# Performance work log

Measured on AMD Instinct MI355X. Metric: run time of the kernel, lower is better.

The kernel has to match this reference:

```python
import jax, jax.numpy as jnp
import numpy as np

T_STEPS = 100
T_EMB = 16
EPS = 1e-8


def sin_emb(t, dim):
    # sinusoidal_time_embedding: [cos(t*f), sin(t*f)] with f = exp(-log(1e4)*i/half)
    half = dim // 2
    freqs = jnp.exp(-jnp.log(jnp.float32(10000.0)) * jnp.arange(half, dtype=jnp.float32) / half)
    a = t.astype(jnp.float32)[:, None] * freqs[None, :]
    return jnp.concatenate([jnp.cos(a), jnp.sin(a)], axis=-1)


def lstm_layer(x_tbf, W_ih, W_hh, b):
    # x_tbf: [T, B, F]; torch gate order i, f, g, o
    B = x_tbf.shape[1]
    H = W_hh.shape[1]

    def step(carry, x_t):
        h, c = carry
        g = x_t @ W_ih.T + h @ W_hh.T + b
        i, f, gg, o = jnp.split(g, 4, axis=-1)
        c = jax.nn.sigmoid(f) * c + jax.nn.sigmoid(i) * jnp.tanh(gg)
        h = jax.nn.sigmoid(o) * jnp.tanh(c)
        return (h, c), h

    z = jnp.zeros((B, H), x_tbf.dtype)
    (h, c), ys = jax.lax.scan(step, (z, z), x_tbf)
    return ys, h


def _forward(x_hist, x_future, y0, turb_idx, pred_steps, init_noise, turb_emb,
             W_ih0, W_hh0, b_ih0, b_hh0, W_ih1, W_hh1, b_ih1, b_hh1,
             W1, b1, W2, b2, W3, b3):
    betas = jnp.linspace(1e-4, 0.02, T_STEPS).astype(jnp.float32)
    alphas = 1.0 - betas
    alpha_bars = jnp.cumprod(alphas)

    B = x_hist.shape[0]
    emb = turb_emb[turb_idx]  # [B, E]
    eh = jnp.broadcast_to(emb[:, None, :], (B, x_hist.shape[1], emb.shape[1]))
    ef = jnp.broadcast_to(emb[:, None, :], (B, x_future.shape[1], emb.shape[1]))
    xh = jnp.concatenate([x_hist, eh], axis=-1).transpose(1, 0, 2)    # [T_in, B, F+E]
    xf = jnp.concatenate([x_future, ef], axis=-1).transpose(1, 0, 2)  # [P, B, exo+E]

    ys0, _ = lstm_layer(xh, W_ih0, W_hh0, b_ih0 + b_hh0)
    _, enc_out = lstm_layer(ys0, W_ih1, W_hh1, b_ih1 + b_hh1)         # [B, H] = h[-1]

    def mlp(x):
        h = jax.nn.relu(x @ W1.T + b1)
        h = jax.nn.relu(h @ W2.T + b2)
        return h @ W3.T + b3

    def ar_step(prev_y, xs):
        exo_t, step, y_init = xs
        cond = jnp.concatenate([enc_out, exo_t, prev_y], axis=1)  # [B, cond_dim]
        h_e = sin_emb(jnp.full((B,), step), T_EMB)

        def dstep(y, t):
            t_e = sin_emb(jnp.full((B,), t), T_EMB)
            eps_hat = mlp(jnp.concatenate([cond, y, t_e, h_e], axis=1))  # [B,1]
            b_t, a_t, ab_t = betas[t], alphas[t], alpha_bars[t]
            pred_x0 = (y - jnp.sqrt(1.0 - ab_t) * eps_hat) / (jnp.sqrt(ab_t) + EPS)
            mean = (y - b_t / (jnp.sqrt(1.0 - ab_t) + EPS) * eps_hat) / (jnp.sqrt(a_t) + EPS)
            # eval mode -> deterministic sampling: posterior noise term is zero
            return jnp.where(t == 0, pred_x0, mean), None

        y, _ = jax.lax.scan(dstep, y_init, jnp.arange(T_STEPS - 1, -1, -1))
        return y, y[:, 0]

    _, seq = jax.lax.scan(ar_step, y0, (xf, jnp.arange(pred_steps), init_noise))
    return seq.T[:, :, None]  # [B, pred_steps, 1]


def setup_inputs() -> dict:
    key = jax.random.key(0)
    ks = list(jax.random.split(key, 24))
    kit = iter(ks)
    B, T_IN, F_IN, EXO, EMB, PRED, HID, NTURB = 1024, 96, 8, 6, 16, 8, 128, 100
    in0 = F_IN + EMB                 # 24
    cond_dim = HID + EXO + EMB + 1   # 151
    in_mlp = cond_dim + 1 + T_EMB + T_EMB  # 184

    def nrm(shape, s=0.05):
        return jax.random.normal(next(kit), shape, jnp.float32) * s

    return {
        'x_hist': jax.random.normal(next(kit), (B, T_IN, F_IN), jnp.float32),
        'x_future': jax.random.normal(next(kit), (B, PRED, EXO), jnp.float32),
        'y0': jnp.zeros((B, 1), jnp.float32),
        'turb_idx': jax.random.randint(next(kit), (B,), 0, NTURB),
        'pred_steps': PRED,
        'init_noise': jax.random.normal(next(kit), (PRED, B, 1), jnp.float32),
        'turb_emb': nrm((NTURB, EMB), 0.1),
        'W_ih0': nrm((4 * HID, in0)), 'W_hh0': nrm((4 * HID, HID)),
        'b_ih0': jnp.zeros((4 * HID,), jnp.float32), 'b_hh0': jnp.zeros((4 * HID,), jnp.float32),
        'W_ih1': nrm((4 * HID, HID)), 'W_hh1': nrm((4 * HID, HID)),
        'b_ih1': jnp.zeros((4 * HID,), jnp.float32), 'b_hh1': jnp.zeros((4 * HID,), jnp.float32),
        'W1': nrm((HID, in_mlp)), 'b1': jnp.zeros((HID,), jnp.float32),
        'W2': nrm((HID, HID)), 'b2': jnp.zeros((HID,), jnp.float32),
        'W3': nrm((1, HID)), 'b3': jnp.zeros((1,), jnp.float32),
    }


def reference(x_hist, x_future, y0, turb_idx, pred_steps, init_noise, turb_emb,
              W_ih0, W_hh0, b_ih0, b_hh0, W_ih1, W_hh1, b_ih1, b_hh1,
              W1, b1, W2, b2, W3, b3):
    return _forward(x_hist, x_future, y0, turb_idx, pred_steps, init_noise, turb_emb,
                    W_ih0, W_hh0, b_ih0, b_hh0, W_ih1, W_hh1, b_ih1, b_hh1,
                    W1, b1, W2, b2, W3, b3)
```

## Files before the change

kernel.cpp:

```cpp
#include <hip/hip_runtime.h>
#include <hip/hip_fp16.h>
#include <stdint.h>


typedef __attribute__((ext_vector_type(2))) _Float16 half2_t;
typedef __attribute__((ext_vector_type(8))) _Float16 v8h;
typedef __attribute__((ext_vector_type(4))) float v4f;

#define DEV __device__ __forceinline__

DEV uint32_t pack2f(float a, float b) {
  __half ha = __float2half_rn(a), hb = __float2half_rn(b);
  return (uint32_t)__half_as_ushort(ha) | ((uint32_t)__half_as_ushort(hb) << 16);
}

DEV float2 up2(uint32_t u) {
  half2_t h = __builtin_bit_cast(half2_t, u);
  return make_float2((float)h.x, (float)h.y);
}

DEV float fast_ex2(float x) {
#if __has_builtin(__builtin_amdgcn_exp2f)
  return __builtin_amdgcn_exp2f(x);
#else
  return exp2f(x);
#endif
}
DEV float fast_rcp(float x) {
#if __has_builtin(__builtin_amdgcn_rcpf)
  return __builtin_amdgcn_rcpf(x);
#else
  return 1.f / x;
#endif
}
DEV float sigm(float x) { return fast_rcp(1.f + fast_ex2(-1.4426950408889634f * x)); }
DEV float tanh_f(float x) {
  return 2.f * fast_rcp(1.f + fast_ex2(-2.8853900817779268f * x)) - 1.f;
}

DEV uint32_t pk_add(uint32_t a, uint32_t b) {
  return __builtin_bit_cast(uint32_t,
      __builtin_bit_cast(half2_t, a) + __builtin_bit_cast(half2_t, b));
}

DEV uint32_t pk_relufma(uint32_t w, uint32_t y, uint32_t b) {
  half2_t r = __builtin_bit_cast(half2_t, w) * __builtin_bit_cast(half2_t, y) +
              __builtin_bit_cast(half2_t, b);
  half2_t z = {(_Float16)0.f, (_Float16)0.f};
#if __has_builtin(__builtin_elementwise_max)
  r = __builtin_elementwise_max(r, z);
#else
  uint32_t u = __builtin_bit_cast(uint32_t, r);
  uint32_t mask = ((u >> 15) & 1u) * 0xFFFFu | ((u >> 31) & 1u) * 0xFFFF0000u;
  r = __builtin_bit_cast(half2_t, u & ~mask);
#endif
  return __builtin_bit_cast(uint32_t, r);
}

DEV uint32_t cvtpk(float y) {
#if __has_builtin(__builtin_amdgcn_cvt_pkrtz)
  return __builtin_bit_cast(uint32_t, __builtin_amdgcn_cvt_pkrtz(y, y));
#else
  return pack2f(y, y);
#endif
}

DEV float rowsum16(float v) {
  int x;
  x = __builtin_amdgcn_update_dpp(0, __builtin_bit_cast(int, v), 0x111, 0xf, 0xf, true);
  v += __builtin_bit_cast(float, x);
  x = __builtin_amdgcn_update_dpp(0, __builtin_bit_cast(int, v), 0x112, 0xf, 0xf, true);
  v += __builtin_bit_cast(float, x);
  x = __builtin_amdgcn_update_dpp(0, __builtin_bit_cast(int, v), 0x114, 0xf, 0xf, true);
  v += __builtin_bit_cast(float, x);
  x = __builtin_amdgcn_update_dpp(0, __builtin_bit_cast(int, v), 0x118, 0xf, 0xf, true);
  v += __builtin_bit_cast(float, x);
  return v;
}

static constexpr size_t OFF_XH  = 0;
static constexpr size_t OFF_W0  = 4718592;
static constexpr size_t OFF_BS0 = 4882432;
static constexpr size_t OFF_W1L = 4884480;
static constexpr size_t OFF_BS1 = 5146624;
static constexpr size_t OFF_W2P = 5148672;
static constexpr size_t OFF_ENC = 5181440;
static constexpr size_t OFF_YS0 = 5705728;

__global__ void k_prep_xh(const float* __restrict__ xh, const int* __restrict__ tix,
                          const float* __restrict__ temb, uint32_t* __restrict__ out) {
  int idx = blockIdx.x * 256 + threadIdx.x;
  if (idx >= 96 * 1024 * 12) return;
  int m = idx % 12;
  int tb = idx / 12;
  int b = tb & 1023, t = tb >> 10;
  int k0 = 2 * m, k1 = k0 + 1;
  float v0 = (k0 < 8) ? xh[(b * 96 + t) * 8 + k0] : temb[tix[b] * 16 + (k0 - 8)];
  float v1 = (k1 < 8) ? xh[(b * 96 + t) * 8 + k1] : temb[tix[b] * 16 + (k1 - 8)];
  out[idx] = pack2f(v0, v1);
}

__global__ void k_prep_w(const float* __restrict__ Wih0, const float* __restrict__ Whh0,
                         const float* __restrict__ bih0, const float* __restrict__ bhh0,
                         const float* __restrict__ Wih1, const float* __restrict__ Whh1,
                         const float* __restrict__ bih1, const float* __restrict__ bhh1,
                         const float* __restrict__ W2,
                         uint32_t* __restrict__ w0p, uint32_t* __restrict__ w1p,
                         uint32_t* __restrict__ w2p, float* __restrict__ bs0,
                         float* __restrict__ bs1) {
  int idx = blockIdx.x * 256 + threadIdx.x;
  if (idx < 40960) {
    int w = idx / 5120;
    int r = idx % 5120;
    int T = r / 1280; r %= 1280;
    int f = r / 256;  r %= 256;
    int l = r >> 2, c = r & 3;
    int m = l & 15, qf = l >> 4;
    int g = (m & 3) * 128 + w * 16 + (m >> 2) * 4 + T;
    int k0 = f * 32 + qf * 8 + 2 * c, k1 = k0 + 1;
    float a = (k0 < 24) ? Wih0[g * 24 + k0] : ((k0 < 152) ? Whh0[g * 128 + k0 - 24] : 0.f);
    float b = (k1 < 24) ? Wih0[g * 24 + k1] : ((k1 < 152) ? Whh0[g * 128 + k1 - 24] : 0.f);
    w0p[idx] = pack2f(a, b);
  } else if (idx < 106496) {
    int i = idx - 40960;
    int w = i / 8192;
    int r = i % 8192;
    int T = r / 2048; r %= 2048;
    int f = r / 256;  r %= 256;
    int l = r >> 2, c = r & 3;
    int m = l & 15, qf = l >> 4;
    int g = (m & 3) * 128 + w * 16 + (m >> 2) * 4 + T;
    int k0 = f * 32 + qf * 8 + 2 * c, k1 = k0 + 1;
    float a = (k0 < 128) ? Wih1[g * 128 + k0] : Whh1[g * 128 + k0 - 128];
    float b = (k1 < 128) ? Wih1[g * 128 + k1] : Whh1[g * 128 + k1 - 128];
    w1p[i] = pack2f(a, b);
  } else if (idx < 114688) {
    int i = idx - 106496;
    w2p[i] = pack2f(W2[2 * i], W2[2 * i + 1]);
  } else if (idx < 115200) {
    int i = idx - 114688;
    bs0[i] = bih0[i] + bhh0[i];
  } else if (idx < 115712) {
    int i = idx - 115200;
    bs1[i] = bih1[i] + bhh1[i];
  }
}

__global__ __launch_bounds__(512, 2) void k_lstm0(const uint32_t* __restrict__ xh16,
                                                  const uint32_t* __restrict__ w0A,
                                                  const float* __restrict__ bs0,
                                                  __half* __restrict__ ys0) {
  __shared__ __align__(16) __half inb[2][16][160];
  const int tid = threadIdx.x;
  const int w = tid >> 6, l = tid & 63;
  const int n = l & 15, ql = l >> 4;
  const int ju = w * 16 + ql * 4;
  const int bbase = blockIdx.x * 16;

  uint4 Af[4][5];
#pragma unroll
  for (int T = 0; T < 4; T++)
#pragma unroll
    for (int f = 0; f < 5; f++)
      Af[T][f] = ((const uint4*)w0A)[((w * 4 + T) * 5 + f) * 64 + l];
  float bias[4][4];
#pragma unroll
  for (int T = 0; T < 4; T++)
#pragma unroll
    for (int r = 0; r < 4; r++) bias[T][r] = bs0[r * 128 + ju + T];

  for (int i = tid; i < 2560; i += 512) ((uint32_t*)inb)[i] = 0u;
  __syncthreads();
  if (tid < 192) {
    int b = tid / 12, m = tid % 12;
    ((uint32_t*)&inb[0][b][0])[m] = xh16[(0 * 1024 + bbase + b) * 12 + m];
  }
  float cst[4] = {0.f, 0.f, 0.f, 0.f};
  __syncthreads();

  for (int t = 0; t < 96; t++) {
    const int cur = t & 1, nxt = cur ^ 1;
    uint32_t sx = 0;
    int sb = 0, sm = 0;
    if (t < 95 && tid < 192) {
      sb = tid / 12; sm = tid % 12;
      sx = xh16[((t + 1) * 1024 + bbase + sb) * 12 + sm];
    }
    v4f acc[4];
#pragma unroll
    for (int T = 0; T < 4; T++) acc[T] = (v4f){0.f, 0.f, 0.f, 0.f};
#pragma unroll
    for (int f = 0; f < 5; f++) {
      uint4 bu = *(const uint4*)&inb[cur][n][f * 32 + ql * 8];
      v8h Bv = __builtin_bit_cast(v8h, bu);
#pragma unroll
      for (int T = 0; T < 4; T++)
        acc[T] = __builtin_amdgcn_mfma_f32_16x16x32_f16(
            __builtin_bit_cast(v8h, Af[T][f]), Bv, acc[T], 0, 0, 0);
    }
    float hv[4];
#pragma unroll
    for (int T = 0; T < 4; T++) {
      float gi = acc[T][0] + bias[T][0];
      float gf = acc[T][1] + bias[T][1];
      float gg = acc[T][2] + bias[T][2];
      float go = acc[T][3] + bias[T][3];
      float c = sigm(gf) * cst[T] + sigm(gi) * tanh_f(gg);
      cst[T] = c;
      hv[T] = sigm(go) * tanh_f(c);
    }
    uint32_t h01 = pack2f(hv[0], hv[1]), h23 = pack2f(hv[2], hv[3]);
    *(uint2*)&inb[nxt][n][24 + ju] = make_uint2(h01, h23);
    *(uint2*)((__half*)ys0 + (size_t)(t * 1024 + bbase + n) * 128 + ju) = make_uint2(h01, h23);
    if (t < 95 && tid < 192) ((uint32_t*)&inb[nxt][sb][0])[sm] = sx;
    __syncthreads();
  }
}

__global__ __launch_bounds__(512, 2) void k_lstm1(const uint32_t* __restrict__ ys0u,
                                                  const uint32_t* __restrict__ w1A,
                                                  const float* __restrict__ bs1,
                                                  float* __restrict__ enc) {
  __shared__ __align__(16) __half inb[2][16][264];
  const int tid = threadIdx.x;
  const int w = tid >> 6, l = tid & 63;
  const int n = l & 15, ql = l >> 4;
  const int ju = w * 16 + ql * 4;
  const int bbase = blockIdx.x * 16;
  const int sb = tid >> 5, sc = tid & 31;

  uint4 Af[4][8];
#pragma unroll
  for (int T = 0; T < 4; T++)
#pragma unroll
    for (int f = 0; f < 8; f++)
      Af[T][f] = ((const uint4*)w1A)[((w * 4 + T) * 8 + f) * 64 + l];
  float bias[4][4];
#pragma unroll
  for (int T = 0; T < 4; T++)
#pragma unroll
    for (int r = 0; r < 4; r++) bias[T][r] = bs1[r * 128 + ju + T];

  for (int i = tid; i < 4224; i += 512) ((uint32_t*)inb)[i] = 0u;
  __syncthreads();
  {
    uint2 v = ((const uint2*)ys0u)[(size_t)(0 * 1024 + bbase + sb) * 32 + sc];
    *(uint2*)&inb[0][sb][sc * 4] = v;
  }
  float cst[4] = {0.f, 0.f, 0.f, 0.f};
  __syncthreads();

  for (int t = 0; t < 96; t++) {
    const int cur = t & 1, nxt = cur ^ 1;
    uint2 sv = make_uint2(0u, 0u);
    if (t < 95)
      sv = ((const uint2*)ys0u)[(size_t)((t + 1) * 1024 + bbase + sb) * 32 + sc];
    v4f acc[4];
#pragma unroll
    for (int T = 0; T < 4; T++) acc[T] = (v4f){0.f, 0.f, 0.f, 0.f};
#pragma unroll
    for (int f = 0; f < 8; f++) {
      uint4 bu = *(const uint4*)&inb[cur][n][f * 32 + ql * 8];
      v8h Bv = __builtin_bit_cast(v8h, bu);
#pragma unroll
      for (int T = 0; T < 4; T++)
        acc[T] = __builtin_amdgcn_mfma_f32_16x16x32_f16(
            __builtin_bit_cast(v8h, Af[T][f]), Bv, acc[T], 0, 0, 0);
    }
    float hv[4];
#pragma unroll
    for (int T = 0; T < 4; T++) {
      float gi = acc[T][0] + bias[T][0];
      float gf = acc[T][1] + bias[T][1];
      float gg = acc[T][2] + bias[T][2];
      float go = acc[T][3] + bias[T][3];
      float c = sigm(gf) * cst[T] + sigm(gi) * tanh_f(gg);
      cst[T] = c;
      hv[T] = sigm(go) * tanh_f(c);
    }
    *(uint2*)&inb[nxt][n][128 + ju] = make_uint2(pack2f(hv[0], hv[1]), pack2f(hv[2], hv[3]));
    if (t < 95) *(uint2*)&inb[nxt][sb][sc * 4] = sv;
    if (t == 95)
      *(float4*)&enc[(size_t)(bbase + n) * 128 + ju] = make_float4(hv[0], hv[1], hv[2], hv[3]);
    __syncthreads();
  }
}

__global__ __launch_bounds__(256, 1) void k_diff(
    const float* __restrict__ xfut, const float* __restrict__ y0,
    const int* __restrict__ tix, const float* __restrict__ noise,
    const float* __restrict__ temb, const float* __restrict__ W1,
    const float* __restrict__ b1, const float* __restrict__ b2,
    const float* __restrict__ W3, const float* __restrict__ b3,
    const uint32_t* __restrict__ w2p, const float* __restrict__ enc,
    float* __restrict__ out) {
  __shared__ uint32_t W1sL[128 * 65];
  __shared__ uint32_t W1xL[128 * 29];
  __shared__ uint32_t encPL[16 * 65];
  __shared__ uint32_t embPL[16 * 9];
  __shared__ float teL[100][16];
  __shared__ float2 ccL[100];
  __shared__ __align__(16) __half tprojL[100 * 128];
  __shared__ __half hprojL[8 * 128];
  __shared__ __align__(16) float partL[2][4][16];
  __shared__ uint32_t encdL[256 * 17];

  const int tid = threadIdx.x;
  const int w = tid >> 6, l = tid & 63;
  const int m = l & 15, q = l >> 4;
  const int bbase = blockIdx.x * 16;

  for (int i = tid; i < 128 * 64; i += 256) {
    int r = i >> 6, c = i & 63;
    W1sL[r * 65 + c] = pack2f(W1[r * 184 + 2 * c], W1[r * 184 + 2 * c + 1]);
  }
  for (int i = tid; i < 128 * 28; i += 256) {
    int r = i / 28, c = i % 28;
    W1xL[r * 29 + c] = pack2f(W1[r * 184 + 128 + 2 * c], W1[r * 184 + 129 + 2 * c]);
  }
  for (int i = tid; i < 16 * 64; i += 256) {
    int bb = i >> 6, c = i & 63;
    encPL[bb * 65 + c] = pack2f(enc[(bbase + bb) * 128 + 2 * c],
                                enc[(bbase + bb) * 128 + 2 * c + 1]);
  }
  for (int i = tid; i < 16 * 8; i += 256) {
    int bb = i >> 3, c = i & 7;
    const float* er = temb + tix[bbase + bb] * 16;
    embPL[bb * 9 + c] = pack2f(er[2 * c], er[2 * c + 1]);
  }
  for (int p = tid; p < 1600; p += 256) {
    int tt = p >> 4, i = p & 15;
    float f = expf(-logf(10000.f) * (float)(i & 7) / 8.f);
    float a = (float)tt * f;
    teL[tt][i] = (i < 8) ? cosf(a) : sinf(a);
  }
  for (int qq = tid; qq < 100; qq += 256) {
    float ab = 1.f, beta = 0.f;
    for (int i = 0; i <= qq; i++) {
      beta = 1e-4f + (0.02f - 1e-4f) * (float)i / 99.f;
      ab *= (1.f - beta);
    }
    float cs, cd;
    if (qq == 0) { cs = sqrtf(1.f - ab); cd = 1.f / (sqrtf(ab) + 1e-8f); }
    else { cs = beta / (sqrtf(1.f - ab) + 1e-8f); cd = 1.f / (sqrtf(1.f - beta) + 1e-8f); }
    ccL[qq] = make_float2(cs, cd);
  }
  __syncthreads();

  {
    int k = tid & 127, hs = tid >> 7;
    float wte[16], whe[16];
#pragma unroll
    for (int i = 0; i < 8; i++) {
      float2 a = up2(W1xL[k * 29 + 12 + i]);
      wte[2 * i] = a.x; wte[2 * i + 1] = a.y;
      float2 bqq = up2(W1xL[k * 29 + 20 + i]);
      whe[2 * i] = bqq.x; whe[2 * i + 1] = bqq.y;
    }
    for (int tt = hs * 50; tt < hs * 50 + 50; tt++) {
      float s = 0.f;
#pragma unroll
      for (int i = 0; i < 16; i++) s += wte[i] * teL[tt][i];
      tprojL[tt * 128 + k] = __float2half_rn(s);
    }
    if (hs == 0) {
      for (int ss = 0; ss < 8; ss++) {
        float s = 0.f;
#pragma unroll
        for (int i = 0; i < 16; i++) s += whe[i] * teL[ss][i];
        hprojL[ss * 128 + k] = __float2half_rn(s);
      }
    }
  }

  for (int pi = 0; pi < 16; pi++) {
    int k0 = (pi >> 2) * 32 + q * 8 + (pi & 3) * 2;
    half2_t a0 = {(_Float16)0.f, (_Float16)0.f};
    half2_t a1 = a0;
    const uint32_t* wr0 = &W1sL[k0 * 65];
    const uint32_t* wr1 = &W1sL[(k0 + 1) * 65];
    const uint32_t* ep = &encPL[m * 65];
#pragma unroll 8
    for (int c = 0; c < 64; c++) {
      half2_t e = __builtin_bit_cast(half2_t, ep[c]);
      a0 += __builtin_bit_cast(half2_t, wr0[c]) * e;
      a1 += __builtin_bit_cast(half2_t, wr1[c]) * e;
    }
#pragma unroll
    for (int c = 0; c < 8; c++) {
      half2_t e = __builtin_bit_cast(half2_t, embPL[m * 9 + c]);
      a0 += __builtin_bit_cast(half2_t, W1xL[k0 * 29 + 3 + c]) * e;
      a1 += __builtin_bit_cast(half2_t, W1xL[(k0 + 1) * 29 + 3 + c]) * e;
    }
    float e0 = b1[k0] + (float)a0.x + (float)a0.y;
    float e1 = b1[k0 + 1] + (float)a1.x + (float)a1.y;
    encdL[tid * 17 + pi] = pack2f(e0, e1);
  }

  uint4 Bf[2][4];
  const uint4* w2u4 = (const uint4*)w2p;
#pragma unroll
  for (int tt = 0; tt < 2; tt++) {
    int n = w * 32 + tt * 16 + m;
#pragma unroll
    for (int f = 0; f < 4; f++) Bf[tt][f] = w2u4[n * 16 + f * 4 + q];
  }
  const float w3v0 = W3[w * 32 + m], w3v1 = W3[w * 32 + 16 + m];
  const float b2v0 = b2[w * 32 + m], b2v1 = b2[w * 32 + 16 + m];
  const float b3v = b3[0];

  uint32_t w1yP[16];
#pragma unroll
  for (int pi = 0; pi < 16; pi++) {
    int k0 = (pi >> 2) * 32 + q * 8 + (pi & 3) * 2;
    uint32_t ua = W1xL[k0 * 29 + 11];
    uint32_t ub = W1xL[(k0 + 1) * 29 + 11];
    w1yP[pi] = (ua >> 16) | (ub & 0xFFFF0000u);
  }

  float prev_y = y0[bbase + m];
  float noi[8];
#pragma unroll
  for (int s = 0; s < 8; s++) noi[s] = noise[s * 1024 + bbase + m];
  __syncthreads();

  int buf = 0;
  for (int s = 0; s < 8; s++) {
    float xf[6];
#pragma unroll
    for (int i = 0; i < 6; i++) xf[i] = xfut[((bbase + m) * 8 + s) * 6 + i];
    uint32_t bph[16];
#pragma unroll
    for (int pi = 0; pi < 16; pi++) {
      int k0 = (pi >> 2) * 32 + q * 8 + (pi & 3) * 2;
      float2 ed = up2(encdL[tid * 17 + pi]);
      float e0 = ed.x, e1 = ed.y;
#pragma unroll
      for (int c = 0; c < 3; c++) {
        float2 w0v = up2(W1xL[k0 * 29 + c]);
        float2 w1v = up2(W1xL[(k0 + 1) * 29 + c]);
        e0 += w0v.x * xf[2 * c] + w0v.y * xf[2 * c + 1];
        e1 += w1v.x * xf[2 * c] + w1v.y * xf[2 * c + 1];
      }
      e0 += up2(W1xL[k0 * 29 + 11]).x * prev_y;
      e1 += up2(W1xL[(k0 + 1) * 29 + 11]).x * prev_y;
      e0 += (float)hprojL[s * 128 + k0];
      e1 += (float)hprojL[s * 128 + k0 + 1];
      bph[pi] = pack2f(e0, e1);
    }

    float y = noi[s];
    uint32_t bt[16];
    {
      const uint4* tb = (const uint4*)(tprojL + 99 * 128 + q * 8);
      uint4 t0 = tb[0], t1 = tb[4], t2 = tb[8], t3 = tb[12];
      bt[0] = pk_add(bph[0], t0.x);  bt[1] = pk_add(bph[1], t0.y);
      bt[2] = pk_add(bph[2], t0.z);  bt[3] = pk_add(bph[3], t0.w);
      bt[4] = pk_add(bph[4], t1.x);  bt[5] = pk_add(bph[5], t1.y);
      bt[6] = pk_add(bph[6], t1.z);  bt[7] = pk_add(bph[7], t1.w);
      bt[8] = pk_add(bph[8], t2.x);  bt[9] = pk_add(bph[9], t2.y);
      bt[10] = pk_add(bph[10], t2.z); bt[11] = pk_add(bph[11], t2.w);
      bt[12] = pk_add(bph[12], t3.x); bt[13] = pk_add(bph[13], t3.y);
      bt[14] = pk_add(bph[14], t3.z); bt[15] = pk_add(bph[15], t3.w);
    }
    float2 ccv = ccL[99];

    for (int t = 99; t >= 0; t--) {
      uint32_t yP = cvtpk(y);
      v4f c0a = {0.f, 0.f, 0.f, 0.f}, c0b = c0a, c1a = c0a, c1b = c0a;
#pragma unroll
      for (int f = 0; f < 4; f++) {
        uint4 au;
        au.x = pk_relufma(w1yP[4 * f + 0], yP, bt[4 * f + 0]);
        au.y = pk_relufma(w1yP[4 * f + 1], yP, bt[4 * f + 1]);
        au.z = pk_relufma(w1yP[4 * f + 2], yP, bt[4 * f + 2]);
        au.w = pk_relufma(w1yP[4 * f + 3], yP, bt[4 * f + 3]);
        v8h A = __builtin_bit_cast(v8h, au);
        if (f & 1) {
          c0b = __builtin_amdgcn_mfma_f32_16x16x32_f16(A, __builtin_bit_cast(v8h, Bf[0][f]), c0b, 0, 0, 0);
          c1b = __builtin_amdgcn_mfma_f32_16x16x32_f16(A, __builtin_bit_cast(v8h, Bf[1][f]), c1b, 0, 0, 0);
        } else {
          c0a = __builtin_amdgcn_mfma_f32_16x16x32_f16(A, __builtin_bit_cast(v8h, Bf[0][f]), c0a, 0, 0, 0);
          c1a = __builtin_amdgcn_mfma_f32_16x16x32_f16(A, __builtin_bit_cast(v8h, Bf[1][f]), c1a, 0, 0, 0);
        }
      }
      const int tn = (t > 0) ? t - 1 : 0;
      const uint4* tb = (const uint4*)(tprojL + tn * 128 + q * 8);
      uint4 t0 = tb[0], t1 = tb[4], t2 = tb[8], t3 = tb[12];
      float2 ccn = ccL[tn];
      v4f c0 = c0a + c0b, c1 = c1a + c1b;
      float pr[4];
#pragma unroll
      for (int r = 0; r < 4; r++) {
        pr[r] = fmaxf(c0[r] + b2v0, 0.f) * w3v0 + fmaxf(c1[r] + b2v1, 0.f) * w3v1;
        pr[r] = rowsum16(pr[r]);
      }
      if ((l & 15) == 15)
        *(float4*)&partL[buf][w][q * 4] = make_float4(pr[0], pr[1], pr[2], pr[3]);
      uint32_t btn[16];
      btn[0] = pk_add(bph[0], t0.x);  btn[1] = pk_add(bph[1], t0.y);
      btn[2] = pk_add(bph[2], t0.z);  btn[3] = pk_add(bph[3], t0.w);
      btn[4] = pk_add(bph[4], t1.x);  btn[5] = pk_add(bph[5], t1.y);
      btn[6] = pk_add(bph[6], t1.z);  btn[7] = pk_add(bph[7], t1.w);
      btn[8] = pk_add(bph[8], t2.x);  btn[9] = pk_add(bph[9], t2.y);
      btn[10] = pk_add(bph[10], t2.z); btn[11] = pk_add(bph[11], t2.w);
      btn[12] = pk_add(bph[12], t3.x); btn[13] = pk_add(bph[13], t3.y);
      btn[14] = pk_add(bph[14], t3.z); btn[15] = pk_add(bph[15], t3.w);
      __syncthreads();
      float eps = b3v + ((partL[buf][0][m] + partL[buf][1][m]) +
                         (partL[buf][2][m] + partL[buf][3][m]));
      y = (y - ccv.x * eps) * ccv.y;
      ccv = ccn;
#pragma unroll
      for (int pi = 0; pi < 16; pi++) bt[pi] = btn[pi];
      buf ^= 1;
    }
    if (w == 0 && l < 16) out[(bbase + l) * 8 + s] = y;
    prev_y = y;
  }
}

extern "C" void kernel_launch(void* const* d_in, const int* in_sizes, int n_in,
                              void* d_out, int out_size, void* d_ws, size_t ws_size,
                              hipStream_t stream) {
  const float* x_hist    = (const float*)d_in[0];
  const float* x_future  = (const float*)d_in[1];
  const float* y0        = (const float*)d_in[2];
  const int*   turb_idx  = (const int*)d_in[3];
  const float* init_noise = (const float*)d_in[5];
  const float* turb_emb  = (const float*)d_in[6];
  const float* W_ih0     = (const float*)d_in[7];
  const float* W_hh0     = (const float*)d_in[8];
  const float* b_ih0     = (const float*)d_in[9];
  const float* b_hh0     = (const float*)d_in[10];
  const float* W_ih1     = (const float*)d_in[11];
  const float* W_hh1     = (const float*)d_in[12];
  const float* b_ih1     = (const float*)d_in[13];
  const float* b_hh1     = (const float*)d_in[14];
  const float* W1        = (const float*)d_in[15];
  const float* b1        = (const float*)d_in[16];
  const float* W2        = (const float*)d_in[17];
  const float* b2        = (const float*)d_in[18];
  const float* W3        = (const float*)d_in[19];
  const float* b3        = (const float*)d_in[20];

  char* ws = (char*)d_ws;
  uint32_t* xh16 = (uint32_t*)(ws + OFF_XH);
  uint32_t* w0p  = (uint32_t*)(ws + OFF_W0);
  float*    bs0  = (float*)(ws + OFF_BS0);
  uint32_t* w1p  = (uint32_t*)(ws + OFF_W1L);
  float*    bs1  = (float*)(ws + OFF_BS1);
  uint32_t* w2p  = (uint32_t*)(ws + OFF_W2P);
  float*    encf = (float*)(ws + OFF_ENC);
  __half*   ys0h = (__half*)(ws + OFF_YS0);

  k_prep_xh<<<4608, 256, 0, stream>>>(x_hist, turb_idx, turb_emb, xh16);
  k_prep_w<<<452, 256, 0, stream>>>(W_ih0, W_hh0, b_ih0, b_hh0,
                                    W_ih1, W_hh1, b_ih1, b_hh1,
                                    W2, w0p, w1p, w2p, bs0, bs1);
  k_lstm0<<<64, 512, 0, stream>>>(xh16, w0p, bs0, ys0h);
  k_lstm1<<<64, 512, 0, stream>>>((const uint32_t*)ys0h, w1p, bs1, encf);
  k_diff<<<64, 256, 0, stream>>>(x_future, y0, turb_idx, init_noise, turb_emb,
                                 W1, b1, b2, W3, b3, w2p, encf, (float*)d_out);
}
```

Measured before the change: 670.3 us.

## Give each wave its own 16-sample batch in diffusion loop, removing block barriers

Result: slower. 889.0 us (+32.6%).

```diff
diff --git a/kernel.cpp b/kernel.cpp
--- a/kernel.cpp
+++ b/kernel.cpp
@@ -63,19 +63,6 @@
 #else
   return pack2f(y, y);
 #endif
-}
-
-DEV float rowsum16(float v) {
-  int x;
-  x = __builtin_amdgcn_update_dpp(0, __builtin_bit_cast(int, v), 0x111, 0xf, 0xf, true);
-  v += __builtin_bit_cast(float, x);
-  x = __builtin_amdgcn_update_dpp(0, __builtin_bit_cast(int, v), 0x112, 0xf, 0xf, true);
-  v += __builtin_bit_cast(float, x);
-  x = __builtin_amdgcn_update_dpp(0, __builtin_bit_cast(int, v), 0x114, 0xf, 0xf, true);
-  v += __builtin_bit_cast(float, x);
-  x = __builtin_amdgcn_update_dpp(0, __builtin_bit_cast(int, v), 0x118, 0xf, 0xf, true);
-  v += __builtin_bit_cast(float, x);
-  return v;
 }
 
 static constexpr size_t OFF_XH  = 0;
@@ -296,19 +283,20 @@
     float* __restrict__ out) {
   __shared__ uint32_t W1sL[128 * 65];
   __shared__ uint32_t W1xL[128 * 29];
-  __shared__ uint32_t encPL[16 * 65];
-  __shared__ uint32_t embPL[16 * 9];
+  __shared__ uint32_t encPL[64 * 65];
+  __shared__ uint32_t embPL[64 * 9];
   __shared__ float teL[100][16];
   __shared__ float2 ccL[100];
   __shared__ __align__(16) __half tprojL[100 * 128];
   __shared__ __half hprojL[8 * 128];
-  __shared__ __align__(16) float partL[2][4][16];
   __shared__ uint32_t encdL[256 * 17];
 
   const int tid = threadIdx.x;
   const int w = tid >> 6, l = tid & 63;
   const int m = l & 15, q = l >> 4;
-  const int bbase = blockIdx.x * 16;
+  const int gbase = blockIdx.x * 64;
+  const int bb = gbase + w * 16;
+  const int wm = w * 16 + m;
 
   for (int i = tid; i < 128 * 64; i += 256) {
     int r = i >> 6, c = i & 63;
@@ -318,15 +306,15 @@
     int r = i / 28, c = i % 28;
     W1xL[r * 29 + c] = pack2f(W1[r * 184 + 128 + 2 * c], W1[r * 184 + 129 + 2 * c]);
   }
-  for (int i = tid; i < 16 * 64; i += 256) {
-    int bb = i >> 6, c = i & 63;
-    encPL[bb * 65 + c] = pack2f(enc[(bbase + bb) * 128 + 2 * c],
-                                enc[(bbase + bb) * 128 + 2 * c + 1]);
-  }
-  for (int i = tid; i < 16 * 8; i += 256) {
-    int bb = i >> 3, c = i & 7;
-    const float* er = temb + tix[bbase + bb] * 16;
-    embPL[bb * 9 + c] = pack2f(er[2 * c], er[2 * c + 1]);
+  for (int i = tid; i < 64 * 64; i += 256) {
+    int bq = i >> 6, c = i & 63;
+    encPL[bq * 65 + c] = pack2f(enc[(gbase + bq) * 128 + 2 * c],
+                                enc[(gbase + bq) * 128 + 2 * c + 1]);
+  }
+  for (int i = tid; i < 64 * 8; i += 256) {
+    int bq = i >> 3, c = i & 7;
+    const float* er = temb + tix[gbase + bq] * 16;
+    embPL[bq * 9 + c] = pack2f(er[2 * c], er[2 * c + 1]);
   }
   for (int p = tid; p < 1600; p += 256) {
     int tt = p >> 4, i = p & 15;
@@ -379,7 +367,7 @@
     half2_t a1 = a0;
     const uint32_t* wr0 = &W1sL[k0 * 65];
     const uint32_t* wr1 = &W1sL[(k0 + 1) * 65];
-    const uint32_t* ep = &encPL[m * 65];
+    const uint32_t* ep = &encPL[wm * 65];
 #pragma unroll 8
     for (int c = 0; c < 64; c++) {
       half2_t e = __builtin_bit_cast(half2_t, ep[c]);
@@ -388,7 +376,7 @@
     }
 #pragma unroll
     for (int c = 0; c < 8; c++) {
-      half2_t e = __builtin_bit_cast(half2_t, embPL[m * 9 + c]);
+      half2_t e = __builtin_bit_cast(half2_t, embPL[wm * 9 + c]);
       a0 += __builtin_bit_cast(half2_t, W1xL[k0 * 29 + 3 + c]) * e;
       a1 += __builtin_bit_cast(half2_t, W1xL[(k0 + 1) * 29 + 3 + c]) * e;
     }
@@ -397,17 +385,22 @@
     encdL[tid * 17 + pi] = pack2f(e0, e1);
   }
 
-  uint4 Bf[2][4];
+  uint4 Bf[8][4];
   const uint4* w2u4 = (const uint4*)w2p;
 #pragma unroll
-  for (int tt = 0; tt < 2; tt++) {
-    int n = w * 32 + tt * 16 + m;
+  for (int tt = 0; tt < 8; tt++) {
+    int n = tt * 16 + m;
 #pragma unroll
     for (int f = 0; f < 4; f++) Bf[tt][f] = w2u4[n * 16 + f * 4 + q];
   }
-  const float w3v0 = W3[w * 32 + m], w3v1 = W3[w * 32 + 16 + m];
-  const float b2v0 = b2[w * 32 + m], b2v1 = b2[w * 32 + 16 + m];
+  v4f b2w[8], w3w[8];
+#pragma unroll
+  for (int tt = 0; tt < 8; tt++) {
+    b2w[tt] = *(const v4f*)&b2[tt * 16 + q * 4];
+    w3w[tt] = *(const v4f*)&W3[tt * 16 + q * 4];
+  }
   const float b3v = b3[0];
+  const int bpaddr = (l ^ 32) << 2;
 
   uint32_t w1yP[16];
 #pragma unroll
@@ -418,18 +411,79 @@
     w1yP[pi] = (ua >> 16) | (ub & 0xFFFF0000u);
   }
 
-  float prev_y = y0[bbase + m];
+  float prev_y = y0[bb + m];
   float noi[8];
 #pragma unroll
-  for (int s = 0; s < 8; s++) noi[s] = noise[s * 1024 + bbase + m];
+  for (int s = 0; s < 8; s++) noi[s] = noise[s * 1024 + bb + m];
   __syncthreads();
 
-  int buf = 0;
+  float y = 0.f;
+  float2 ccv = make_float2(0.f, 0.f);
+  uint32_t bph[16], btA[16], btB[16];
+
+#define DSTEP(t_, BTC, BTN)                                                    \
+  do {                                                                         \
+    const uint32_t yP = cvtpk(y);                                              \
+    v4f acc[8];                                                                \
+    {                                                                          \
+      uint4 au;                                                                \
+      au.x = pk_relufma(w1yP[0], yP, BTC[0]);                                  \
+      au.y = pk_relufma(w1yP[1], yP, BTC[1]);                                  \
+      au.z = pk_relufma(w1yP[2], yP, BTC[2]);                                  \
+      au.w = pk_relufma(w1yP[3], yP, BTC[3]);                                  \
+      v8h Av = __builtin_bit_cast(v8h, au);                                    \
+      _Pragma("unroll")                                                        \
+      for (int tt = 0; tt < 8; tt++)                                           \
+        acc[tt] = __builtin_amdgcn_mfma_f32_16x16x32_f16(                      \
+            __builtin_bit_cast(v8h, Bf[tt][0]), Av, b2w[tt], 0, 0, 0);         \
+    }                                                                          \
+    _Pragma("unroll")                                                          \
+    for (int f = 1; f < 4; f++) {                                              \
+      uint4 au;                                                                \
+      au.x = pk_relufma(w1yP[4 * f + 0], yP, BTC[4 * f + 0]);                  \
+      au.y = pk_relufma(w1yP[4 * f + 1], yP, BTC[4 * f + 1]);                  \
+      au.z = pk_relufma(w1yP[4 * f + 2], yP, BTC[4 * f + 2]);                  \
+      au.w = pk_relufma(w1yP[4 * f + 3], yP, BTC[4 * f + 3]);                  \
+      v8h Av = __builtin_bit_cast(v8h, au);                                    \
+      _Pragma("unroll")                                                        \
+      for (int tt = 0; tt < 8; tt++)                                           \
+        acc[tt] = __builtin_amdgcn_mfma_f32_16x16x32_f16(                      \
+            __builtin_bit_cast(v8h, Bf[tt][f]), Av, acc[tt], 0, 0, 0);         \
+    }                                                                          \
+    const int tn_ = ((t_) > 0) ? (t_) - 1 : 0;                                 \
+    const uint4* tb_ = (const uint4*)(tprojL + tn_ * 128 + q * 8);             \
+    uint4 t0 = tb_[0], t1 = tb_[4], t2 = tb_[8], t3 = tb_[12];                 \
+    float2 ccn_ = ccL[tn_];                                                    \
+    float stt[8];                                                              \
+    _Pragma("unroll")                                                          \
+    for (int tt = 0; tt < 8; tt++) {                                           \
+      float e0 = fmaxf(acc[tt][0], 0.f), e1 = fmaxf(acc[tt][1], 0.f);          \
+      float e2 = fmaxf(acc[tt][2], 0.f), e3 = fmaxf(acc[tt][3], 0.f);          \
+      stt[tt] = (e0 * w3w[tt][0] + e1 * w3w[tt][1]) +                          \
+                (e2 * w3w[tt][2] + e3 * w3w[tt][3]);                           \
+    }                                                                          \
+    float sv = ((stt[0] + stt[1]) + (stt[2] + stt[3])) +                       \
+               ((stt[4] + stt[5]) + (stt[6] + stt[7]));                        \
+    sv += __builtin_bit_cast(float, __builtin_amdgcn_ds_swizzle(               \
+              __builtin_bit_cast(int, sv), 0x401F));                           \
+    sv += __builtin_bit_cast(float, __builtin_amdgcn_ds_bpermute(              \
+              bpaddr, __builtin_bit_cast(int, sv)));                           \
+    y = (y - ccv.x * (b3v + sv)) * ccv.y;                                      \
+    ccv = ccn_;                                                                \
+    BTN[0] = pk_add(bph[0], t0.x);   BTN[1] = pk_add(bph[1], t0.y);            \
+    BTN[2] = pk_add(bph[2], t0.z);   BTN[3] = pk_add(bph[3], t0.w);            \
+    BTN[4] = pk_add(bph[4], t1.x);   BTN[5] = pk_add(bph[5], t1.y);            \
+    BTN[6] = pk_add(bph[6], t1.z);   BTN[7] = pk_add(bph[7], t1.w);            \
+    BTN[8] = pk_add(bph[8], t2.x);   BTN[9] = pk_add(bph[9], t2.y);            \
+    BTN[10] = pk_add(bph[10], t2.z); BTN[11] = pk_add(bph[11], t2.w);          \
+    BTN[12] = pk_add(bph[12], t3.x); BTN[13] = pk_add(bph[13], t3.y);          \
+    BTN[14] = pk_add(bph[14], t3.z); BTN[15] = pk_add(bph[15], t3.w);          \
+  } while (0)
+
   for (int s = 0; s < 8; s++) {
     float xf[6];
 #pragma unroll
-    for (int i = 0; i < 6; i++) xf[i] = xfut[((bbase + m) * 8 + s) * 6 + i];
-    uint32_t bph[16];
+    for (int i = 0; i < 6; i++) xf[i] = xfut[((bb + m) * 8 + s) * 6 + i];
 #pragma unroll
     for (int pi = 0; pi < 16; pi++) {
       int k0 = (pi >> 2) * 32 + q * 8 + (pi & 3) * 2;
@@ -449,75 +503,30 @@
       bph[pi] = pack2f(e0, e1);
     }
 
-    float y = noi[s];
-    uint32_t bt[16];
+    y = noi[s];
     {
       const uint4* tb = (const uint4*)(tprojL + 99 * 128 + q * 8);
       uint4 t0 = tb[0], t1 = tb[4], t2 = tb[8], t3 = tb[12];
-      bt[0] = pk_add(bph[0], t0.x);  bt[1] = pk_add(bph[1], t0.y);
-      bt[2] = pk_add(bph[2], t0.z);  bt[3] = pk_add(bph[3], t0.w);
-      bt[4] = pk_add(bph[4], t1.x);  bt[5] = pk_add(bph[5], t1.y);
-      bt[6] = pk_add(bph[6], t1.z);  bt[7] = pk_add(bph[7], t1.w);
-      bt[8] = pk_add(bph[8], t2.x);  bt[9] = pk_add(bph[9], t2.y);
-      bt[10] = pk_add(bph[10], t2.z); bt[11] = pk_add(bph[11], t2.w);
-      bt[12] = pk_add(bph[12], t3.x); bt[13] = pk_add(bph[13], t3.y);
-      bt[14] = pk_add(bph[14], t3.z); bt[15] = pk_add(bph[15], t3.w);
-    }
-    float2 ccv = ccL[99];
-
-    for (int t = 99; t >= 0; t--) {
-      uint32_t yP = cvtpk(y);
-      v4f c0a = {0.f, 0.f, 0.f, 0.f}, c0b = c0a, c1a = c0a, c1b = c0a;
-#pragma unroll
-      for (int f = 0; f < 4; f++) {
-        uint4 au;
-        au.x = pk_relufma(w1yP[4 * f + 0], yP, bt[4 * f + 0]);
-        au.y = pk_relufma(w1yP[4 * f + 1], yP, bt[4 * f + 1]);
-        au.z = pk_relufma(w1yP[4 * f + 2], yP, bt[4 * f + 2]);
-        au.w = pk_relufma(w1yP[4 * f + 3], yP, bt[4 * f + 3]);
-        v8h A = __builtin_bit_cast(v8h, au);
-        if (f & 1) {
-          c0b = __builtin_amdgcn_mfma_f32_16x16x32_f16(A, __builtin_bit_cast(v8h, Bf[0][f]), c0b, 0, 0, 0);
-          c1b = __builtin_amdgcn_mfma_f32_16x16x32_f16(A, __builtin_bit_cast(v8h, Bf[1][f]), c1b, 0, 0, 0);
-        } else {
-          c0a = __builtin_amdgcn_mfma_f32_16x16x32_f16(A, __builtin_bit_cast(v8h, Bf[0][f]), c0a, 0, 0, 0);
-          c1a = __builtin_amdgcn_mfma_f32_16x16x32_f16(A, __builtin_bit_cast(v8h, Bf[1][f]), c1a, 0, 0, 0);
-        }
-      }
-      const int tn = (t > 0) ? t - 1 : 0;
-      const uint4* tb = (const uint4*)(tprojL + tn * 128 + q * 8);
-      uint4 t0 = tb[0], t1 = tb[4], t2 = tb[8], t3 = tb[12];
-      float2 ccn = ccL[tn];
-      v4f c0 = c0a + c0b, c1 = c1a + c1b;
-      float pr[4];
-#pragma unroll
-      for (int r = 0; r < 4; r++) {
-        pr[r] = fmaxf(c0[r] + b2v0, 0.f) * w3v0 + fmaxf(c1[r] + b2v1, 0.f) * w3v1;
-        pr[r] = rowsum16(pr[r]);
-      }
-      if ((l & 15) == 15)
-        *(float4*)&partL[buf][w][q * 4] = make_float4(pr[0], pr[1], pr[2], pr[3]);
-      uint32_t btn[16];
-      btn[0] = pk_add(bph[0], t0.x);  btn[1] = pk_add(bph[1], t0.y);
-      btn[2] = pk_add(bph[2], t0.z);  btn[3] = pk_add(bph[3], t0.w);
-      btn[4] = pk_add(bph[4], t1.x);  btn[5] = pk_add(bph[5], t1.y);
-      btn[6] = pk_add(bph[6], t1.z);  btn[7] = pk_add(bph[7], t1.w);
-      btn[8] = pk_add(bph[8], t2.x);  btn[9] = pk_add(bph[9], t2.y);
-      btn[10] = pk_add(bph[10], t2.z); btn[11] = pk_add(bph[11], t2.w);
-      btn[12] = pk_add(bph[12], t3.x); btn[13] = pk_add(bph[13], t3.y);
-      btn[14] = pk_add(bph[14], t3.z); btn[15] = pk_add(bph[15], t3.w);
-      __syncthreads();
-      float eps = b3v + ((partL[buf][0][m] + partL[buf][1][m]) +
-                         (partL[buf][2][m] + partL[buf][3][m]));
-      y = (y - ccv.x * eps) * ccv.y;
-      ccv = ccn;
-#pragma unroll
-      for (int pi = 0; pi < 16; pi++) bt[pi] = btn[pi];
-      buf ^= 1;
-    }
-    if (w == 0 && l < 16) out[(bbase + l) * 8 + s] = y;
+      btA[0] = pk_add(bph[0], t0.x);   btA[1] = pk_add(bph[1], t0.y);
+      btA[2] = pk_add(bph[2], t0.z);   btA[3] = pk_add(bph[3], t0.w);
+      btA[4] = pk_add(bph[4], t1.x);   btA[5] = pk_add(bph[5], t1.y);
+      btA[6] = pk_add(bph[6], t1.z);   btA[7] = pk_add(bph[7], t1.w);
+      btA[8] = pk_add(bph[8], t2.x);   btA[9] = pk_add(bph[9], t2.y);
+      btA[10] = pk_add(bph[10], t2.z); btA[11] = pk_add(bph[11], t2.w);
+      btA[12] = pk_add(bph[12], t3.x); btA[13] = pk_add(bph[13], t3.y);
+      btA[14] = pk_add(bph[14], t3.z); btA[15] = pk_add(bph[15], t3.w);
+    }
+    ccv = ccL[99];
+
+    for (int it = 0; it < 50; it++) {
+      DSTEP(99 - 2 * it, btA, btB);
+      DSTEP(98 - 2 * it, btB, btA);
+    }
+
+    if (l < 16) out[(bb + l) * 8 + s] = y;
     prev_y = y;
   }
+#undef DSTEP
 }
 
 extern "C" void kernel_launch(void* const* d_in, const int* in_sizes, int n_in,
@@ -560,6 +569,6 @@
                                     W2, w0p, w1p, w2p, bs0, bs1);
   k_lstm0<<<64, 512, 0, stream>>>(xh16, w0p, bs0, ys0h);
   k_lstm1<<<64, 512, 0, stream>>>((const uint32_t*)ys0h, w1p, bs1, encf);
-  k_diff<<<64, 256, 0, stream>>>(x_future, y0, turb_idx, init_noise, turb_emb,
+  k_diff<<<16, 256, 0, stream>>>(x_future, y0, turb_idx, init_noise, turb_emb,
                                  W1, b1, b2, W3, b3, w2p, encf, (float*)d_out);
 }
```
